# Kernel optimization log

Measured on AMD Instinct MI355X. Metric: run time of the kernel, lower is better.

The kernel has to match this reference:

```python
import jax, jax.numpy as jnp
from jax import lax
import numpy as np


def _qlayer(x, theta):
    """Simulate QLayer: RX(x_i) encoder + trainable RX(theta_i) per wire
    (they commute -> single RX(x_i+theta_i) on |0>), then ring of CNOTs,
    then <Z> on each wire.  x: (B, n) float, theta: (n,). Returns (B, n)."""
    B, n = x.shape
    a = x + theta[None, :]
    c = jnp.cos(a * 0.5)
    s = jnp.sin(a * 0.5)
    # RX(a)|0> = [cos(a/2), -i sin(a/2)] per wire -> product state
    amps = jnp.stack([c + 0j, -1j * s], axis=-1)  # (B, n, 2) complex64
    state = amps[:, 0]  # (B, 2)
    for w in range(1, n):
        state = state[..., None] * amps[:, w].reshape((B,) + (1,) * w + (2,))
    # state: (B, 2, 2, ..., 2), axis w+1 == wire w
    for ctrl in range(n):
        tgt = (ctrl + 1) % n
        s0 = jnp.take(state, 0, axis=ctrl + 1)   # control = 0 block
        s1 = jnp.take(state, 1, axis=ctrl + 1)   # control = 1 block
        t_ax = tgt + 1 if tgt < ctrl else tgt    # target axis after removing ctrl axis
        s1 = jnp.flip(s1, axis=t_ax)             # X on target
        state = jnp.stack([s0, s1], axis=ctrl + 1)
    p = state.real ** 2 + state.imag ** 2
    axes = tuple(range(1, n + 1))
    zs = []
    for w in range(n):
        other = tuple(ax for ax in axes if ax != w + 1)
        pw = jnp.sum(p, axis=other)              # (B, 2)
        zs.append(pw[:, 0] - pw[:, 1])           # <Z_w> = P(0) - P(1)
    return jnp.stack(zs, axis=1)


def setup_inputs() -> dict:
    key = jax.random.key(0)
    ks = jax.random.split(key, 13)
    T, B, D, NQ = 64, 256, 512, 6
    lim = 1.0 / np.sqrt(D + NQ)

    def lin(k):
        k1, k2 = jax.random.split(k)
        W = jax.random.uniform(k1, (D + NQ, NQ), jnp.float32, -lim, lim)
        b = jax.random.uniform(k2, (NQ,), jnp.float32, -lim, lim)
        return W, b

    Wf, bf = lin(ks[0]); Wi, bi = lin(ks[1]); Wu, bu = lin(ks[2]); Wo, bo = lin(ks[3])
    theta_f = jax.random.normal(ks[4], (NQ,), jnp.float32) * 0.1
    theta_i = jax.random.normal(ks[5], (NQ,), jnp.float32) * 0.1
    theta_u = jax.random.normal(ks[6], (NQ,), jnp.float32) * 0.1
    theta_o = jax.random.normal(ks[7], (NQ,), jnp.float32) * 0.1
    inputs = jax.random.normal(ks[8], (T, B, D), jnp.float32)
    return {"inputs": inputs,
            "Wf": Wf, "bf": bf, "Wi": Wi, "bi": bi,
            "Wu": Wu, "bu": bu, "Wo": Wo, "bo": bo,
            "theta_f": theta_f, "theta_i": theta_i,
            "theta_u": theta_u, "theta_o": theta_o}


def reference(inputs, Wf, bf, Wi, bi, Wu, bu, Wo, bo,
              theta_f, theta_i, theta_u, theta_o):
    B = inputs.shape[1]
    NQ = theta_f.shape[0]  # hidden_dim == n_qubits
    h0 = jnp.zeros((B, NQ), inputs.dtype)
    c0 = jnp.zeros((B, NQ), inputs.dtype)

    def step(carry, x):
        hx, cx = carry
        comb = jnp.concatenate([x, hx], axis=1)          # (B, D+NQ)
        f = jax.nn.sigmoid(_qlayer(comb @ Wf + bf, theta_f))
        i = jax.nn.sigmoid(_qlayer(comb @ Wi + bi, theta_i))
        g = jnp.tanh(_qlayer(comb @ Wu + bu, theta_u))
        o = jax.nn.sigmoid(_qlayer(comb @ Wo + bo, theta_o))
        cx2 = f * cx + i * g
        hx2 = o * jnp.tanh(cx2)
        return (hx2, cx2), hx2

    (hx, cx), outputs = lax.scan(step, (h0, c0), inputs)  # outputs: (T, B, NQ)
    return outputs, hx, cx
```

## Files before the change

### kernel.cpp

```cpp
#include <hip/hip_runtime.h>


typedef float v2f __attribute__((ext_vector_type(2)));

__device__ __forceinline__ float fast_rcp(float x) { return __builtin_amdgcn_rcpf(x); }

template <int CTRL>
__device__ __forceinline__ float dpp_add(float x) {
    int t = __builtin_amdgcn_mov_dpp(__float_as_int(x), CTRL, 0xF, 0xF, true);
    return x + __int_as_float(t);
}

template <int G>
__device__ __forceinline__ float quad_bcast(float v) {
    int i = __builtin_amdgcn_mov_dpp(__float_as_int(v), G * 0x55, 0xF, 0xF, true);
    return __int_as_float(i);
}

__global__ __launch_bounds__(512, 4) void gemm_pre(
    const float* __restrict__ X,
    const float* __restrict__ Wf, const float* __restrict__ bf,
    const float* __restrict__ Wi, const float* __restrict__ bi,
    const float* __restrict__ Wu, const float* __restrict__ bu,
    const float* __restrict__ Wo, const float* __restrict__ bo,
    const float* __restrict__ thf, const float* __restrict__ thi,
    const float* __restrict__ thu, const float* __restrict__ tho,
    float* __restrict__ pre)
{
    __shared__ float W_lds[12800];

    const int tid  = threadIdx.x;
    const int w    = tid >> 6;
    const int lane = tid & 63;
    const int rg   = w >> 1;
    const int cg   = w & 1;
    const int rowbase = blockIdx.x * 16;

    {
        const int k = tid;
        #pragma unroll
        for (int g = 0; g < 4; ++g) {
            const float* Wp = (g==0)?Wf:(g==1)?Wi:(g==2)?Wu:Wo;
            const float2* s = (const float2*)(Wp + k*6);
            float2 s0 = s[0], s1 = s[1], s2 = s[2];
            float* d = W_lds + k*25 + g*6;
            d[0] = s0.x; d[1] = s0.y; d[2] = s1.x;
            d[3] = s1.y; d[4] = s2.x; d[5] = s2.y;
        }
    }
    __syncthreads();

    v2f acc[4][6];
    #pragma unroll
    for (int r = 0; r < 4; ++r)
        #pragma unroll
        for (int p = 0; p < 6; ++p) acc[r][p] = (v2f){0.f, 0.f};

    const float* Xr0 = X + (rowbase + rg*4)*512 + lane;
    const int colbase = cg*12;

    float pa[4];
    #pragma unroll
    for (int r = 0; r < 4; ++r) pa[r] = Xr0[r*512];

    #pragma unroll
    for (int kb = 0; kb < 512; kb += 64) {
        const float* Wrow = W_lds + (kb + lane)*25 + colbase;
        float a0 = pa[0], a1 = pa[1], a2 = pa[2], a3 = pa[3];
        if (kb < 448) {
            #pragma unroll
            for (int r = 0; r < 4; ++r) pa[r] = Xr0[kb + 64 + r*512];
        }
        #pragma unroll
        for (int p = 0; p < 6; ++p) {
            float wa = Wrow[p];
            float wb = Wrow[p + 6];
            v2f wv = (v2f){wa, wb};
            acc[0][p] = __builtin_elementwise_fma((v2f){a0,a0}, wv, acc[0][p]);
            acc[1][p] = __builtin_elementwise_fma((v2f){a1,a1}, wv, acc[1][p]);
            acc[2][p] = __builtin_elementwise_fma((v2f){a2,a2}, wv, acc[2][p]);
            acc[3][p] = __builtin_elementwise_fma((v2f){a3,a3}, wv, acc[3][p]);
        }
    }

    #pragma unroll
    for (int r = 0; r < 4; ++r)
        #pragma unroll
        for (int p = 0; p < 6; ++p) {
            float x = acc[r][p].x;
            x = dpp_add<0xB1>(x);
            x = dpp_add<0x4E>(x);
            acc[r][p].x = x;
            float y = acc[r][p].y;
            y = dpp_add<0xB1>(y);
            y = dpp_add<0x4E>(y);
            acc[r][p].y = y;
        }

    #define ACCV(v) ((((v) % 12) < 6) ? acc[(v)/12][(v)%6].x \
                                      : acc[(v)/12][(v)%6].y)
    const int j = lane & 3;
    const int q = lane >> 2;
    const bool j1 = (j & 1) != 0, j2 = (j & 2) != 0;
    float sel[12];
    #pragma unroll
    for (int i = 0; i < 12; ++i) {
        float c0 = ACCV(i*4 + 0), c1 = ACCV(i*4 + 1);
        float c2 = ACCV(i*4 + 2), c3 = ACCV(i*4 + 3);
        float lo = j1 ? c1 : c0;
        float hi = j1 ? c3 : c2;
        sel[i] = j2 ? hi : lo;
    }
    #undef ACCV

    __syncthreads();
    #pragma unroll
    for (int i = 0; i < 12; ++i) {
        W_lds[(w*48 + i*4 + j)*16 + q] = sel[i];
    }
    __syncthreads();

    if (tid < 384) {
        int o = tid;
        int ww = o / 48, v = o - ww*48;
        int rr = v / 12, ph = v - rr*12;
        const float4* rp = (const float4*)(W_lds + (ww*48 + v)*16);
        float4 r0 = rp[0], r1 = rp[1], r2 = rp[2], r3 = rp[3];
        float s = ((r0.x+r0.y)+(r0.z+r0.w)) + ((r1.x+r1.y)+(r1.z+r1.w))
                + ((r2.x+r2.y)+(r2.z+r2.w)) + ((r3.x+r3.y)+(r3.z+r3.w));
        int col = (ww & 1)*12 + ph;
        int g = col / 6, jg = col - g*6;
        const float* bb = (g==0)?bf:(g==1)?bi:(g==2)?bu:bo;
        const float* tt = (g==0)?thf:(g==1)?thi:(g==2)?thu:tho;
        s += bb[jg] + tt[jg];
        int row = rowbase + (ww >> 1)*4 + rr;
        pre[row*24 + col] = s;
    }
}

__global__ __launch_bounds__(64, 1) void qlstm_scan(
    const float* __restrict__ pre,
    const float* __restrict__ Wf, const float* __restrict__ Wi,
    const float* __restrict__ Wu, const float* __restrict__ Wo,
    float* __restrict__ out)
{
    const int lane = threadIdx.x;
    const int bl   = lane >> 2;
    const int g    = lane & 3;
    const int b    = blockIdx.x * 16 + bl;

    const float* Wg = (g==0)?Wf:(g==1)?Wi:(g==2)?Wu:Wo;
    v2f Wh2[6][3];
    #pragma unroll
    for (int j = 0; j < 6; ++j)
        #pragma unroll
        for (int p = 0; p < 3; ++p)
            Wh2[j][p] = (v2f){Wg[(512 + j)*6 + 2*p], Wg[(512 + j)*6 + 2*p + 1]};

    const float c0 = (g==2) ? 0.f        : 0.5f;
    const float n0 = (g==2) ? 15.f       : 0.25f;
    const float n1 = (g==2) ? 1.f        : -0.020833333f;
    const float n2 = (g==2) ? 0.f        : 0.0020833333f;
    const float d0 = (g==2) ? 15.f       : 1.f;
    const float d1 = (g==2) ? 6.f        : 0.f;

    float h[6], c[6];
    #pragma unroll
    for (int w = 0; w < 6; ++w) { h[w] = 0.f; c[w] = 0.f; }

    const float* pb = pre + b*24 + g*6;
    v2f x0 = *(const v2f*)(pb);
    v2f x1 = *(const v2f*)(pb + 2);
    v2f x2 = *(const v2f*)(pb + 4);
    v2f n0v = *(const v2f*)(pb + 256*24);
    v2f n1v = *(const v2f*)(pb + 256*24 + 2);
    v2f n2v = *(const v2f*)(pb + 256*24 + 4);

    for (int t = 0; t < 64; ++t) {
        v2f a2[3] = {x0, x1, x2};
        x0 = n0v; x1 = n1v; x2 = n2v;
        int tn = (t < 62) ? (t + 2) : 63;
        const float* pn = pre + (tn*256 + b)*24 + g*6;
        n0v = *(const v2f*)(pn);
        n1v = *(const v2f*)(pn + 2);
        n2v = *(const v2f*)(pn + 4);

        #pragma unroll
        for (int j = 0; j < 6; ++j) {
            v2f hj = (v2f){h[j], h[j]};
            #pragma unroll
            for (int p = 0; p < 3; ++p)
                a2[p] = __builtin_elementwise_fma(hj, Wh2[j][p], a2[p]);
        }

        float C[6];
        C[0] = __cosf(a2[0].x); C[1] = __cosf(a2[0].y);
        C[2] = __cosf(a2[1].x); C[3] = __cosf(a2[1].y);
        C[4] = __cosf(a2[2].x); C[5] = __cosf(a2[2].y);

        float p01 = C[0]*C[1], p23 = C[2]*C[3], p45 = C[4]*C[5];
        float z[6];
        z[1] = p01;
        z[2] = p01*C[2];
        z[3] = p01*p23;
        z[4] = z[3]*C[4];
        z[5] = z[3]*p45;
        z[0] = C[1]*(p23*p45);

        float act[6];
        #pragma unroll
        for (int w = 0; w < 6; ++w) {
            float y   = z[w]*z[w];
            float num = fmaf(y, fmaf(y, n2, n1), n0);
            float den = fmaf(y, d1, d0);
            act[w] = fmaf(z[w]*num, fast_rcp(den), c0);
        }

        float F[6], I[6], U[6], O[6];
        #pragma unroll
        for (int w = 0; w < 6; ++w) {
            F[w] = quad_bcast<0>(act[w]);
            I[w] = quad_bcast<1>(act[w]);
            U[w] = quad_bcast<2>(act[w]);
            O[w] = quad_bcast<3>(act[w]);
        }

        #pragma unroll
        for (int w = 0; w < 6; ++w) {
            c[w] = fmaf(F[w], c[w], I[w]*U[w]);
            float y   = c[w]*c[w];
            float num = fmaf(y, fmaf(y, 1.f, 105.f), 945.f);
            float den = fmaf(y, fmaf(y, 15.f, 420.f), 945.f);
            float tc  = c[w]*num*fast_rcp(den);
            h[w] = O[w]*tc;
        }

        if (g < 3) {
            float2 v;
            v.x = (g==0) ? h[0] : (g==1) ? h[2] : h[4];
            v.y = (g==0) ? h[1] : (g==1) ? h[3] : h[5];
            *(float2*)(out + (t*256 + b)*6 + g*2) = v;
        }
    }

    if (g < 3) {
        float2 v;
        v.x = (g==0) ? h[0] : (g==1) ? h[2] : h[4];
        v.y = (g==0) ? h[1] : (g==1) ? h[3] : h[5];
        *(float2*)(out + 64*256*6 + b*6 + g*2) = v;
        float2 u;
        u.x = (g==0) ? c[0] : (g==1) ? c[2] : c[4];
        u.y = (g==0) ? c[1] : (g==1) ? c[3] : c[5];
        *(float2*)(out + 64*256*6 + 256*6 + b*6 + g*2) = u;
    }
}

extern "C" void kernel_launch(void* const* d_in, const int* in_sizes, int n_in,
                              void* d_out, int out_size, void* d_ws, size_t ws_size,
                              hipStream_t stream) {
    const float* X   = (const float*)d_in[0];
    const float* Wf  = (const float*)d_in[1];
    const float* bf_ = (const float*)d_in[2];
    const float* Wi  = (const float*)d_in[3];
    const float* bi_ = (const float*)d_in[4];
    const float* Wu  = (const float*)d_in[5];
    const float* bu_ = (const float*)d_in[6];
    const float* Wo  = (const float*)d_in[7];
    const float* bo_ = (const float*)d_in[8];
    const float* thf = (const float*)d_in[9];
    const float* thi = (const float*)d_in[10];
    const float* thu = (const float*)d_in[11];
    const float* tho = (const float*)d_in[12];

    float* pre = (float*)d_ws;
    float* out = (float*)d_out;

    gemm_pre<<<1024, 512, 0, stream>>>(X, Wf, bf_, Wi, bi_, Wu, bu_, Wo, bo_,
                                       thf, thi, thu, tho, pre);
    qlstm_scan<<<16, 64, 0, stream>>>(pre, Wf, Wi, Wu, Wo, out);
}
```

Baseline: 137.6 us.

## Fuse GEMM and recurrent scan into one kernel with per-timestep completion flags

Merges the input-projection GEMM and the sequential QLSTM scan into a single launch. The first 16 blocks run the scan and spin-wait on per-timestep atomic counters, while the remaining blocks compute projections and signal completion. The goal is to overlap the recurrent scan with the GEMM and remove the second kernel launch. It adds a memset, spin-waiting, and a dependence on scan blocks being co-resident with producer blocks; scan blocks also hold 512-thread slots while only 64 threads do work.

```diff
diff --git a/kernel.cpp b/kernel.cpp
--- a/kernel.cpp
+++ b/kernel.cpp
@@ -17,7 +17,7 @@
     return __int_as_float(i);
 }
 
-__global__ __launch_bounds__(512, 4) void gemm_pre(
+__global__ __launch_bounds__(512, 4) void qlstm_fused(
     const float* __restrict__ X,
     const float* __restrict__ Wf, const float* __restrict__ bf,
     const float* __restrict__ Wi, const float* __restrict__ bi,
@@ -25,129 +25,133 @@
     const float* __restrict__ Wo, const float* __restrict__ bo,
     const float* __restrict__ thf, const float* __restrict__ thi,
     const float* __restrict__ thu, const float* __restrict__ tho,
-    float* __restrict__ pre)
+    int* __restrict__ doneF, float* __restrict__ pre,
+    float* __restrict__ out)
 {
     __shared__ float W_lds[12800];
-
-    const int tid  = threadIdx.x;
-    const int w    = tid >> 6;
-    const int lane = tid & 63;
-    const int rg   = w >> 1;
-    const int cg   = w & 1;
-    const int rowbase = blockIdx.x * 16;
-
-    {
-        const int k = tid;
-        #pragma unroll
-        for (int g = 0; g < 4; ++g) {
-            const float* Wp = (g==0)?Wf:(g==1)?Wi:(g==2)?Wu:Wo;
-            const float2* s = (const float2*)(Wp + k*6);
-            float2 s0 = s[0], s1 = s[1], s2 = s[2];
-            float* d = W_lds + k*25 + g*6;
-            d[0] = s0.x; d[1] = s0.y; d[2] = s1.x;
-            d[3] = s1.y; d[4] = s2.x; d[5] = s2.y;
-        }
+    const int bid = blockIdx.x;
+    const int tid = threadIdx.x;
+
+    if (bid >= 16) {
+        const int w    = tid >> 6;
+        const int lane = tid & 63;
+        const int rg   = w >> 1;
+        const int cg   = w & 1;
+        const int rowbase = (bid - 16) * 16;
+
+        {
+            const int k = tid;
+            #pragma unroll
+            for (int g = 0; g < 4; ++g) {
+                const float* Wp = (g==0)?Wf:(g==1)?Wi:(g==2)?Wu:Wo;
+                const float2* s = (const float2*)(Wp + k*6);
+                float2 s0 = s[0], s1 = s[1], s2 = s[2];
+                float* d = W_lds + k*25 + g*6;
+                d[0] = s0.x; d[1] = s0.y; d[2] = s1.x;
+                d[3] = s1.y; d[4] = s2.x; d[5] = s2.y;
+            }
+        }
+        __syncthreads();
+
+        v2f acc[4][6];
+        #pragma unroll
+        for (int r = 0; r < 4; ++r)
+            #pragma unroll
+            for (int p = 0; p < 6; ++p) acc[r][p] = (v2f){0.f, 0.f};
+
+        const float* Xr0 = X + (rowbase + rg*4)*512 + lane;
+        const int colbase = cg*12;
+
+        float pa[4];
+        #pragma unroll
+        for (int r = 0; r < 4; ++r) pa[r] = Xr0[r*512];
+
+        #pragma unroll
+        for (int kb = 0; kb < 512; kb += 64) {
+            const float* Wrow = W_lds + (kb + lane)*25 + colbase;
+            float a0 = pa[0], a1 = pa[1], a2 = pa[2], a3 = pa[3];
+            if (kb < 448) {
+                #pragma unroll
+                for (int r = 0; r < 4; ++r) pa[r] = Xr0[kb + 64 + r*512];
+            }
+            #pragma unroll
+            for (int p = 0; p < 6; ++p) {
+                float wa = Wrow[p];
+                float wb = Wrow[p + 6];
+                v2f wv = (v2f){wa, wb};
+                acc[0][p] = __builtin_elementwise_fma((v2f){a0,a0}, wv, acc[0][p]);
+                acc[1][p] = __builtin_elementwise_fma((v2f){a1,a1}, wv, acc[1][p]);
+                acc[2][p] = __builtin_elementwise_fma((v2f){a2,a2}, wv, acc[2][p]);
+                acc[3][p] = __builtin_elementwise_fma((v2f){a3,a3}, wv, acc[3][p]);
+            }
+        }
+
+        #pragma unroll
+        for (int r = 0; r < 4; ++r)
+            #pragma unroll
+            for (int p = 0; p < 6; ++p) {
+                float x = acc[r][p].x;
+                x = dpp_add<0xB1>(x);
+                x = dpp_add<0x4E>(x);
+                acc[r][p].x = x;
+                float y = acc[r][p].y;
+                y = dpp_add<0xB1>(y);
+                y = dpp_add<0x4E>(y);
+                acc[r][p].y = y;
+            }
+
+        #define ACCV(v) ((((v) % 12) < 6) ? acc[(v)/12][(v)%6].x \
+                                          : acc[(v)/12][(v)%6].y)
+        const int j = lane & 3;
+        const int q = lane >> 2;
+        const bool j1 = (j & 1) != 0, j2 = (j & 2) != 0;
+        float sel[12];
+        #pragma unroll
+        for (int i = 0; i < 12; ++i) {
+            float c0 = ACCV(i*4 + 0), c1 = ACCV(i*4 + 1);
+            float c2 = ACCV(i*4 + 2), c3 = ACCV(i*4 + 3);
+            float lo = j1 ? c1 : c0;
+            float hi = j1 ? c3 : c2;
+            sel[i] = j2 ? hi : lo;
+        }
+        #undef ACCV
+
+        __syncthreads();
+        #pragma unroll
+        for (int i = 0; i < 12; ++i)
+            W_lds[(w*48 + i*4 + j)*16 + q] = sel[i];
+        __syncthreads();
+
+        if (tid < 384) {
+            int o = tid;
+            int ww = o / 48, v = o - ww*48;
+            int rr = v / 12, ph = v - rr*12;
+            const float4* rp = (const float4*)(W_lds + (ww*48 + v)*16);
+            float4 r0 = rp[0], r1 = rp[1], r2 = rp[2], r3 = rp[3];
+            float s = ((r0.x+r0.y)+(r0.z+r0.w)) + ((r1.x+r1.y)+(r1.z+r1.w))
+                    + ((r2.x+r2.y)+(r2.z+r2.w)) + ((r3.x+r3.y)+(r3.z+r3.w));
+            int col = (ww & 1)*12 + ph;
+            int g = col / 6, jg = col - g*6;
+            const float* bb = (g==0)?bf:(g==1)?bi:(g==2)?bu:bo;
+            const float* tt = (g==0)?thf:(g==1)?thi:(g==2)?thu:tho;
+            s += bb[jg] + tt[jg];
+            int row = rowbase + (ww >> 1)*4 + rr;
+            pre[row*24 + col] = s;
+        }
+
+        __syncthreads();
+        if (tid == 0) {
+            __threadfence();
+            atomicAdd(&doneF[(bid - 16) >> 4], 1);
+        }
+        return;
     }
-    __syncthreads();
-
-    v2f acc[4][6];
-    #pragma unroll
-    for (int r = 0; r < 4; ++r)
-        #pragma unroll
-        for (int p = 0; p < 6; ++p) acc[r][p] = (v2f){0.f, 0.f};
-
-    const float* Xr0 = X + (rowbase + rg*4)*512 + lane;
-    const int colbase = cg*12;
-
-    float pa[4];
-    #pragma unroll
-    for (int r = 0; r < 4; ++r) pa[r] = Xr0[r*512];
-
-    #pragma unroll
-    for (int kb = 0; kb < 512; kb += 64) {
-        const float* Wrow = W_lds + (kb + lane)*25 + colbase;
-        float a0 = pa[0], a1 = pa[1], a2 = pa[2], a3 = pa[3];
-        if (kb < 448) {
-            #pragma unroll
-            for (int r = 0; r < 4; ++r) pa[r] = Xr0[kb + 64 + r*512];
-        }
-        #pragma unroll
-        for (int p = 0; p < 6; ++p) {
-            float wa = Wrow[p];
-            float wb = Wrow[p + 6];
-            v2f wv = (v2f){wa, wb};
-            acc[0][p] = __builtin_elementwise_fma((v2f){a0,a0}, wv, acc[0][p]);
-            acc[1][p] = __builtin_elementwise_fma((v2f){a1,a1}, wv, acc[1][p]);
-            acc[2][p] = __builtin_elementwise_fma((v2f){a2,a2}, wv, acc[2][p]);
-            acc[3][p] = __builtin_elementwise_fma((v2f){a3,a3}, wv, acc[3][p]);
-        }
-    }
-
-    #pragma unroll
-    for (int r = 0; r < 4; ++r)
-        #pragma unroll
-        for (int p = 0; p < 6; ++p) {
-            float x = acc[r][p].x;
-            x = dpp_add<0xB1>(x);
-            x = dpp_add<0x4E>(x);
-            acc[r][p].x = x;
-            float y = acc[r][p].y;
-            y = dpp_add<0xB1>(y);
-            y = dpp_add<0x4E>(y);
-            acc[r][p].y = y;
-        }
-
-    #define ACCV(v) ((((v) % 12) < 6) ? acc[(v)/12][(v)%6].x \
-                                      : acc[(v)/12][(v)%6].y)
-    const int j = lane & 3;
-    const int q = lane >> 2;
-    const bool j1 = (j & 1) != 0, j2 = (j & 2) != 0;
-    float sel[12];
-    #pragma unroll
-    for (int i = 0; i < 12; ++i) {
-        float c0 = ACCV(i*4 + 0), c1 = ACCV(i*4 + 1);
-        float c2 = ACCV(i*4 + 2), c3 = ACCV(i*4 + 3);
-        float lo = j1 ? c1 : c0;
-        float hi = j1 ? c3 : c2;
-        sel[i] = j2 ? hi : lo;
-    }
-    #undef ACCV
-
-    __syncthreads();
-    #pragma unroll
-    for (int i = 0; i < 12; ++i) {
-        W_lds[(w*48 + i*4 + j)*16 + q] = sel[i];
-    }
-    __syncthreads();
-
-    if (tid < 384) {
-        int o = tid;
-        int ww = o / 48, v = o - ww*48;
-        int rr = v / 12, ph = v - rr*12;
-        const float4* rp = (const float4*)(W_lds + (ww*48 + v)*16);
-        float4 r0 = rp[0], r1 = rp[1], r2 = rp[2], r3 = rp[3];
-        float s = ((r0.x+r0.y)+(r0.z+r0.w)) + ((r1.x+r1.y)+(r1.z+r1.w))
-                + ((r2.x+r2.y)+(r2.z+r2.w)) + ((r3.x+r3.y)+(r3.z+r3.w));
-        int col = (ww & 1)*12 + ph;
-        int g = col / 6, jg = col - g*6;
-        const float* bb = (g==0)?bf:(g==1)?bi:(g==2)?bu:bo;
-        const float* tt = (g==0)?thf:(g==1)?thi:(g==2)?thu:tho;
-        s += bb[jg] + tt[jg];
-        int row = rowbase + (ww >> 1)*4 + rr;
-        pre[row*24 + col] = s;
-    }
-}
-
-__global__ __launch_bounds__(64, 1) void qlstm_scan(
-    const float* __restrict__ pre,
-    const float* __restrict__ Wf, const float* __restrict__ Wi,
-    const float* __restrict__ Wu, const float* __restrict__ Wo,
-    float* __restrict__ out)
-{
-    const int lane = threadIdx.x;
+
+    if (tid >= 64) return;
+    const int lane = tid;
     const int bl   = lane >> 2;
     const int g    = lane & 3;
-    const int b    = blockIdx.x * 16 + bl;
+    const int b    = bid * 16 + bl;
 
     const float* Wg = (g==0)?Wf:(g==1)?Wi:(g==2)?Wu:Wo;
     v2f Wh2[6][3];
@@ -157,16 +161,22 @@
         for (int p = 0; p < 3; ++p)
             Wh2[j][p] = (v2f){Wg[(512 + j)*6 + 2*p], Wg[(512 + j)*6 + 2*p + 1]};
 
-    const float c0 = (g==2) ? 0.f        : 0.5f;
-    const float n0 = (g==2) ? 15.f       : 0.25f;
-    const float n1 = (g==2) ? 1.f        : -0.020833333f;
-    const float n2 = (g==2) ? 0.f        : 0.0020833333f;
-    const float d0 = (g==2) ? 15.f       : 1.f;
-    const float d1 = (g==2) ? 6.f        : 0.f;
+    const float c0 = (g==2) ? 0.f  : 0.5f;
+    const float n0 = (g==2) ? 15.f : 0.25f;
+    const float n1 = (g==2) ? 1.f  : -0.020833333f;
+    const float n2 = (g==2) ? 0.f  : 0.0020833333f;
+    const float d0 = (g==2) ? 15.f : 1.f;
+    const float d1 = (g==2) ? 6.f  : 0.f;
 
     float h[6], c[6];
     #pragma unroll
     for (int w = 0; w < 6; ++w) { h[w] = 0.f; c[w] = 0.f; }
+
+    for (int tt = 0; tt <= 9; ++tt)
+        while (__hip_atomic_load(doneF + tt, __ATOMIC_RELAXED,
+                                 __HIP_MEMORY_SCOPE_AGENT) < 16)
+            __builtin_amdgcn_s_sleep(2);
+    __threadfence();
 
     const float* pb = pre + b*24 + g*6;
     v2f x0 = *(const v2f*)(pb);
@@ -177,6 +187,15 @@
     v2f n2v = *(const v2f*)(pb + 256*24 + 4);
 
     for (int t = 0; t < 64; ++t) {
+        if ((t & 7) == 0 && t > 0) {
+            int hi = t + 9; if (hi > 63) hi = 63;
+            for (int tt = t + 2; tt <= hi; ++tt)
+                while (__hip_atomic_load(doneF + tt, __ATOMIC_RELAXED,
+                                         __HIP_MEMORY_SCOPE_AGENT) < 16)
+                    __builtin_amdgcn_s_sleep(2);
+            __threadfence();
+        }
+
         v2f a2[3] = {x0, x1, x2};
         x0 = n0v; x1 = n1v; x2 = n2v;
         int tn = (t < 62) ? (t + 2) : 63;
@@ -272,10 +291,12 @@
     const float* thu = (const float*)d_in[11];
     const float* tho = (const float*)d_in[12];
 
-    float* pre = (float*)d_ws;
-    float* out = (float*)d_out;
-
-    gemm_pre<<<1024, 512, 0, stream>>>(X, Wf, bf_, Wi, bi_, Wu, bu_, Wo, bo_,
-                                       thf, thi, thu, tho, pre);
-    qlstm_scan<<<16, 64, 0, stream>>>(pre, Wf, Wi, Wu, Wo, out);
+    int*   doneF = (int*)d_ws;
+    float* pre   = (float*)d_ws + 64;
+    float* out   = (float*)d_out;
+
+    hipMemsetAsync(d_ws, 0, 256, stream);
+    qlstm_fused<<<1040, 512, 0, stream>>>(X, Wf, bf_, Wi, bi_, Wu, bu_,
+                                          Wo, bo_, thf, thi, thu, tho,
+                                          doneF, pre, out);
 }
```

After: 174.9 us. 1.27x slower.
